# Performance work log

Hardware: AMD Instinct MI355X
Metric: run time of the kernel (lower is better)

## Reference

```python
import jax, jax.numpy as jnp
import numpy as np

N, E, F_IN, C, H12, H3, NCLS = 10000, 160000, 50, 256, 4, 6, 121


def gat_conv(x, src, dst, W, a_src, a_dst, b, heads, out_ch, concat, n):
    # x: [n, f_in]; W: [f_in, heads*out_ch]; a_*: [heads, out_ch]; src/dst: [e]
    h = (x @ W).reshape(n, heads, out_ch)
    # per-edge attention logits, LeakyReLU(0.2) as in PyG GATConv
    alpha = jax.nn.leaky_relu((h * a_src).sum(-1)[src] + (h * a_dst).sum(-1)[dst], 0.2)  # [e, heads]
    # segment softmax over incoming edges of each destination node
    amax = jax.ops.segment_max(alpha, dst, num_segments=n)
    ex = jnp.exp(alpha - amax[dst])
    denom = jax.ops.segment_sum(ex, dst, num_segments=n)
    w = ex / (denom[dst] + 1e-16)
    out = jax.ops.segment_sum(h[src] * w[..., None], dst, num_segments=n)  # [n, heads, out_ch]
    out = out.reshape(n, heads * out_ch) if concat else out.mean(axis=1)
    return out + b


def setup_inputs() -> dict:
    key = jax.random.key(0)
    ks = jax.random.split(key, 22)
    s = 0.05
    nrm = lambda k, shp: jax.random.normal(k, shp, jnp.float32) * s
    D = C * H12  # 1024
    return {
        "x": jax.random.normal(ks[0], (N, F_IN), jnp.float32),
        "edge_index": jax.random.randint(ks[1], (2, E), 0, N, dtype=jnp.int32),
        "W1": nrm(ks[2], (F_IN, H12 * C)), "a_src1": nrm(ks[3], (H12, C)), "a_dst1": nrm(ks[4], (H12, C)), "b1": jnp.zeros((H12 * C,), jnp.float32),
        "lW1": nrm(ks[5], (F_IN, D)), "lb1": jnp.zeros((D,), jnp.float32),
        "W2": nrm(ks[6], (D, H12 * C)), "a_src2": nrm(ks[7], (H12, C)), "a_dst2": nrm(ks[8], (H12, C)), "b2": jnp.zeros((H12 * C,), jnp.float32),
        "lW2": nrm(ks[9], (D, D)), "lb2": jnp.zeros((D,), jnp.float32),
        "W3": nrm(ks[10], (D, H3 * NCLS)), "a_src3": nrm(ks[11], (H3, NCLS)), "a_dst3": nrm(ks[12], (H3, NCLS)), "b3": jnp.zeros((NCLS,), jnp.float32),
        "lW3": nrm(ks[13], (D, NCLS)), "lb3": jnp.zeros((NCLS,), jnp.float32),
    }


def reference(x, edge_index, W1, a_src1, a_dst1, b1, lW1, lb1,
              W2, a_src2, a_dst2, b2, lW2, lb2,
              W3, a_src3, a_dst3, b3, lW3, lb3):
    n = x.shape[0]
    loop = jnp.arange(n, dtype=edge_index.dtype)  # self loops (PyG default)
    src = jnp.concatenate([edge_index[0], loop])
    dst = jnp.concatenate([edge_index[1], loop])
    h = jax.nn.elu(gat_conv(x, src, dst, W1, a_src1, a_dst1, b1, H12, C, True, n) + x @ lW1 + lb1)
    h = jax.nn.elu(gat_conv(h, src, dst, W2, a_src2, a_dst2, b2, H12, C, True, n) + h @ lW2 + lb2)
    return gat_conv(h, src, dst, W3, a_src3, a_dst3, b3, H3, NCLS, False, n) + h @ lW3 + lb3
```

## Files before the change

kernel.cpp:

```cpp
#include <hip/hip_runtime.h>
#include <cstdint>
#include <cstddef>

#define NN 10000
#define EE 160000
#define EN_ (EE + NN)
#define MPAD 10112
#define MT 79
#define CAP 128

typedef short s16x8 __attribute__((ext_vector_type(8)));
typedef float f32x4 __attribute__((ext_vector_type(4)));
typedef unsigned short u16;
typedef unsigned char u8;

__device__ __forceinline__ u16 f2bf(float f) {
  uint32_t u = __float_as_uint(f);
  uint32_t r = (u + 0x7fffu + ((u >> 16) & 1u)) >> 16;
  return (u16)r;
}
__device__ __forceinline__ float b2f(u16 u) {
  return __uint_as_float(((uint32_t)u) << 16);
}
__device__ __forceinline__ float b2f_lo(uint32_t p) { return __uint_as_float(p << 16); }
__device__ __forceinline__ float b2f_hi(uint32_t p) { return __uint_as_float(p & 0xffff0000u); }
__device__ __forceinline__ float lrelu02(float x) { return x > 0.f ? x : 0.2f * x; }
__device__ __forceinline__ float eluf(float x) { return x > 0.f ? x : (__expf(x) - 1.f); }
__device__ __forceinline__ u8 f2fp8(float v) {
  v = fminf(fmaxf(v, -448.f), 448.f);
  return (u8)(__builtin_amdgcn_cvt_pk_fp8_f32(v, v, 0, false) & 0xff);
}

__global__ void k_count(const int* __restrict__ ei, int* __restrict__ cnt) {
  int e = blockIdx.x * blockDim.x + threadIdx.x;
  if (e >= EN_) return;
  int d = (e < EE) ? ei[EE + e] : (e - EE);
  atomicAdd(&cnt[d], 1);
}

__global__ __launch_bounds__(1024) void k_scan(const int* __restrict__ cnt, int* __restrict__ off) {
  __shared__ int sums[1024];
  int t = threadIdx.x;
  const int per = (NN + 1023) / 1024;
  int base = t * per;
  int local = 0;
  for (int j = 0; j < per; ++j) {
    int idx = base + j;
    if (idx < NN) local += cnt[idx];
  }
  sums[t] = local;
  __syncthreads();
  for (int s = 1; s < 1024; s <<= 1) {
    int v = (t >= s) ? sums[t - s] : 0;
    __syncthreads();
    sums[t] += v;
    __syncthreads();
  }
  int run = (t == 0) ? 0 : sums[t - 1];
  for (int j = 0; j < per; ++j) {
    int idx = base + j;
    if (idx < NN) { off[idx] = run; run += cnt[idx]; }
  }
  if (t == 1023) off[NN] = EN_;
}

__global__ void k_fill(const int* __restrict__ ei, const int* __restrict__ off,
                       int* __restrict__ cursor, int* __restrict__ csr_src) {
  int e = blockIdx.x * blockDim.x + threadIdx.x;
  if (e >= EN_) return;
  int s, d;
  if (e < EE) { s = ei[e]; d = ei[EE + e]; } else { s = d = e - EE; }
  int p = atomicAdd(&cursor[d], 1);
  csr_src[off[d] + p] = s;
}

#define PREP_BLOCKS 3490
__global__ __launch_bounds__(256) void k_prep(
    const float* __restrict__ x, u16* __restrict__ xb,
    const float* __restrict__ W1, const float* __restrict__ lW1,
    const float* __restrict__ W2, const float* __restrict__ lW2,
    const float* __restrict__ W3, const float* __restrict__ lW3,
    u16* __restrict__ wtc1, u16* __restrict__ wtc2, u16* __restrict__ wtc3,
    const float* __restrict__ lb1, const float* __restrict__ lb2,
    const float* __restrict__ lb3, float* __restrict__ fb,
    u16* __restrict__ bufX, int* __restrict__ cnt) {
  int b = blockIdx.x, t = threadIdx.x;
  if (b < 768) {
    const float* W; u16* Bt; int K, N, Kpad, nb, kb;
    if (b < 16)       { W = W1;  Bt = wtc1;                       K = 50;   N = 1024; Kpad = 64;   nb = b;      kb = 0; }
    else if (b < 32)  { W = lW1; Bt = wtc1 + (size_t)1024 * 64;   K = 50;   N = 1024; Kpad = 64;   nb = b - 16; kb = 0; }
    else if (b < 288) { int r = b - 32;  W = W2;  Bt = wtc2;                         K = 1024; N = 1024; Kpad = 1024; nb = r & 15; kb = r >> 4; }
    else if (b < 544) { int r = b - 288; W = lW2; Bt = wtc2 + (size_t)1024 * 1024;   K = 1024; N = 1024; Kpad = 1024; nb = r & 15; kb = r >> 4; }
    else if (b < 736) { int r = b - 544; W = W3;  Bt = wtc3;                         K = 1024; N = 726;  Kpad = 1024; nb = r % 12; kb = r / 12; }
    else              { int r = b - 736; W = lW3; Bt = wtc3 + (size_t)768 * 1024;    K = 1024; N = 121;  Kpad = 1024; nb = r & 1;  kb = r >> 1; }
    __shared__ float tile[64][65];
    int kbase = kb * 64, nbase = nb * 64;
    int nl = t & 63, kl0 = t >> 6;
#pragma unroll
    for (int j = 0; j < 16; ++j) {
      int k = kbase + kl0 + j * 4, n = nbase + nl;
      tile[kl0 + j * 4][nl] = (k < K && n < N) ? W[(size_t)k * N + n] : 0.f;
    }
    __syncthreads();
    int nr = t >> 2, kc = (t & 3) * 16;
    uint32_t pk[8];
#pragma unroll
    for (int j = 0; j < 8; ++j) {
      pk[j] = (uint32_t)f2bf(tile[kc + 2 * j][nr]) | ((uint32_t)f2bf(tile[kc + 2 * j + 1][nr]) << 16);
    }
    uint4* dst = (uint4*)(Bt + (size_t)(nbase + nr) * Kpad + kbase + kc);
    dst[0] = make_uint4(pk[0], pk[1], pk[2], pk[3]);
    dst[1] = make_uint4(pk[4], pk[5], pk[6], pk[7]);
  } else if (b < 3296) {
    int idx = (b - 768) * 256 + t;
    if (idx < MPAD * 64) {
      int m = idx >> 6, k = idx & 63;
      xb[idx] = f2bf((m < NN && k < 50) ? x[m * 50 + k] : 0.f);
    }
  } else if (b < 3352) {
    int idx = (b - 3296) * 256 + t;
    ((uint4*)(bufX + (size_t)NN * 1024))[idx] = make_uint4(0, 0, 0, 0);
  } else if (b < 3470) {
    int idx = (b - 3352) * 256 + t;
    if (idx < 3 * NN + 1) cnt[idx] = 0;
  } else {
    int idx = (b - 3470) * 256 + t;
    if (idx < 4992) {
      float v = 0.f;
      if (idx < 2048)      { if (idx >= 1024) v = lb1[idx - 1024]; }
      else if (idx < 4096) { int j = idx - 2048; if (j >= 1024) v = lb2[j - 1024]; }
      else                 { int j = idx - 4096; if (j >= 768 && j < 889) v = lb3[j - 768]; }
      fb[idx] = v;
    }
  }
}

template <int OUT_S_BF16>
__global__ __launch_bounds__(256) void k_gemm_fused(
    const u16* __restrict__ A, const u16* __restrict__ Bt,
    const float* __restrict__ fbias,
    u8* __restrict__ outH, int ldH,
    void* __restrict__ outS, int ldS, int nsplit, int nrealS,
    int M, int Kpad, int NS) {
  __shared__ __align__(16) u16 lA[128 * 64];
  __shared__ __align__(16) u16 lB[128 * 64];
  int bid = blockIdx.x;
  int xcd = bid & 7, seq = bid >> 3;
  int nIdx = seq % NS, mloc = seq / NS;
  int mIdx = mloc * 8 + xcd;
  if (mIdx >= MT) return;
  int bm = mIdx * 128, bn = nIdx * 128;

  int t = threadIdx.x;
  int wave = t >> 6, lane = t & 63;
  int wm = (wave >> 1) * 64, wn = (wave & 1) * 64;

  f32x4 acc[4][4];
#pragma unroll
  for (int i = 0; i < 4; ++i)
#pragma unroll
    for (int j = 0; j < 4; ++j)
#pragma unroll
      for (int r = 0; r < 4; ++r) acc[i][j][r] = 0.f;

  int row = lane & 15, quad = lane >> 4;

  for (int k0 = 0; k0 < Kpad; k0 += 64) {
#pragma unroll
    for (int is = 0; is < 4; ++is) {
      int L = is * 256 + t;
      int m = L >> 3, c = L & 7;
      int j = c ^ (m & 7);
      const u16* gpA = A + (size_t)(bm + m) * Kpad + k0 + j * 8;
      const u16* gpB = Bt + (size_t)(bn + m) * Kpad + k0 + j * 8;
      u16* lpA = lA + (size_t)(is * 256 + wave * 64) * 8;
      u16* lpB = lB + (size_t)(is * 256 + wave * 64) * 8;
      __builtin_amdgcn_global_load_lds(
          (const __attribute__((address_space(1))) void*)gpA,
          (__attribute__((address_space(3))) void*)lpA, 16, 0, 0);
      __builtin_amdgcn_global_load_lds(
          (const __attribute__((address_space(1))) void*)gpB,
          (__attribute__((address_space(3))) void*)lpB, 16, 0, 0);
    }
    __syncthreads();

#pragma unroll
    for (int kk = 0; kk < 2; ++kk) {
      s16x8 af[4], bf[4];
#pragma unroll
      for (int mi = 0; mi < 4; ++mi) {
        int m = wm + mi * 16 + row;
        int c = (kk * 4 + quad) ^ (m & 7);
        af[mi] = *(const s16x8*)&lA[m * 64 + c * 8];
      }
#pragma unroll
      for (int ni = 0; ni < 4; ++ni) {
        int n = wn + ni * 16 + row;
        int c = (kk * 4 + quad) ^ (n & 7);
        bf[ni] = *(const s16x8*)&lB[n * 64 + c * 8];
      }
#pragma unroll
      for (int mi = 0; mi < 4; ++mi)
#pragma unroll
        for (int ni = 0; ni < 4; ++ni)
          acc[mi][ni] = __builtin_amdgcn_mfma_f32_16x16x32_bf16(af[mi], bf[ni], acc[mi][ni], 0, 0, 0);
    }
    __syncthreads();
  }

  int col = lane & 15, qr = (lane >> 4) * 4;
  bool isH = bn < nsplit;
#pragma unroll
  for (int mi = 0; mi < 4; ++mi) {
#pragma unroll
    for (int r = 0; r < 4; ++r) {
      int m = bm + wm + mi * 16 + qr + r;
      if (m >= M) continue;
#pragma unroll
      for (int ni = 0; ni < 4; ++ni) {
        int n = bn + wn + ni * 16 + col;
        float v = acc[mi][ni][r] + fbias[n];
        if (isH) {
          outH[(size_t)m * ldH + n] = f2fp8(v);
        } else {
          int c = n - nsplit;
          if (c < nrealS) {
            if (OUT_S_BF16) ((u16*)outS)[(size_t)m * ldS + c] = f2bf(v);
            else ((float*)outS)[(size_t)m * ldS + c] = v;
          }
        }
      }
    }
  }
}

__global__ void k_scores256(const u8* __restrict__ h, const float* __restrict__ a_src,
                            const float* __restrict__ a_dst, float* __restrict__ as_,
                            float* __restrict__ ad_) {
  int wid = (blockIdx.x * blockDim.x + threadIdx.x) >> 6;
  int lane = threadIdx.x & 63;
  if (wid >= NN * 4) return;
  int i = wid >> 2, hh = wid & 3;
  int pk = *(const int*)(h + (size_t)i * 1024 + hh * 256 + 4 * lane);
  float4 av = *(const float4*)(a_src + hh * 256 + 4 * lane);
  float4 dv = *(const float4*)(a_dst + hh * 256 + 4 * lane);
  float x0 = __builtin_amdgcn_cvt_f32_fp8(pk, 0);
  float x1 = __builtin_amdgcn_cvt_f32_fp8(pk, 1);
  float x2 = __builtin_amdgcn_cvt_f32_fp8(pk, 2);
  float x3 = __builtin_amdgcn_cvt_f32_fp8(pk, 3);
  float s1 = x0 * av.x + x1 * av.y + x2 * av.z + x3 * av.w;
  float s2 = x0 * dv.x + x1 * dv.y + x2 * dv.z + x3 * dv.w;
#pragma unroll
  for (int o = 32; o; o >>= 1) {
    s1 += __shfl_down(s1, o);
    s2 += __shfl_down(s2, o);
  }
  if (lane == 0) { as_[wid] = s1; ad_[wid] = s2; }
}

__global__ void k_scores(const u8* __restrict__ h, const float* __restrict__ a_src,
                         const float* __restrict__ a_dst, float* __restrict__ as_,
                         float* __restrict__ ad_, int H, int C, int ld) {
  int wid = (blockIdx.x * blockDim.x + threadIdx.x) >> 6;
  int lane = threadIdx.x & 63;
  if (wid >= NN * H) return;
  int i = wid / H, hh = wid - i * H;
  const u8* hp = h + (size_t)i * ld + hh * C;
  const float* sp = a_src + hh * C;
  const float* dp = a_dst + hh * C;
  float s1 = 0.f, s2 = 0.f;
  for (int c = lane; c < C; c += 64) {
    float v = __builtin_amdgcn_cvt_f32_fp8((int)hp[c], 0);
    s1 += v * sp[c];
    s2 += v * dp[c];
  }
#pragma unroll
  for (int o = 32; o; o >>= 1) {
    s1 += __shfl_down(s1, o);
    s2 += __shfl_down(s2, o);
  }
  if (lane == 0) { as_[wid] = s1; ad_[wid] = s2; }
}

__global__ __launch_bounds__(256) void k_agg_cat(
    const u8* __restrict__ h, const float* __restrict__ as_, const float* __restrict__ ad_,
    const int* __restrict__ off, const int* __restrict__ csr_src,
    const float* __restrict__ bias, const u16* __restrict__ skip, u16* __restrict__ outx) {
  const int F = 1024;
  int i = blockIdx.x, t = threadIdx.x;
  int start = off[i], end = off[i + 1];
  int wave = t >> 6, lane = t & 63;
  __shared__ int src_s[CAP];
  __shared__ float a_s[CAP][4];
  __shared__ float nm_s[4];
  float4 adv = *(const float4*)(ad_ + (size_t)i * 4);
  int hj = wave;
  float m_old = -1e30f;
  float denom = 0.f;
  float acc0 = 0.f, acc1 = 0.f, acc2 = 0.f, acc3 = 0.f;
  for (int e0 = start; e0 < end; e0 += CAP) {
    int ne = min(CAP, end - e0);
    __syncthreads();
    for (int j = t; j < ne; j += 256) {
      int s = csr_src[e0 + j];
      src_s[j] = s;
      float4 av = *(const float4*)(as_ + (size_t)s * 4);
      a_s[j][0] = lrelu02(av.x + adv.x);
      a_s[j][1] = lrelu02(av.y + adv.y);
      a_s[j][2] = lrelu02(av.z + adv.z);
      a_s[j][3] = lrelu02(av.w + adv.w);
    }
    __syncthreads();
    float cm = -1e30f;
    for (int j = lane; j < ne; j += 64) cm = fmaxf(cm, a_s[j][hj]);
#pragma unroll
    for (int o = 32; o; o >>= 1) cm = fmaxf(cm, __shfl_down(cm, o));
    if (lane == 0) nm_s[hj] = fmaxf(m_old, cm);
    __syncthreads();
    float nm0 = nm_s[0], nm1 = nm_s[1], nm2 = nm_s[2], nm3 = nm_s[3];
    for (int j = t; j < ne; j += 256) {
      a_s[j][0] = __expf(a_s[j][0] - nm0);
      a_s[j][1] = __expf(a_s[j][1] - nm1);
      a_s[j][2] = __expf(a_s[j][2] - nm2);
      a_s[j][3] = __expf(a_s[j][3] - nm3);
    }
    __syncthreads();
    float cd = 0.f;
    for (int j = lane; j < ne; j += 64) cd += a_s[j][hj];
#pragma unroll
    for (int o = 32; o; o >>= 1) cd += __shfl_down(cd, o);
    cd = __shfl(cd, 0);
    float nm = nm_s[hj];
    float rs = __expf(m_old - nm);
    acc0 *= rs; acc1 *= rs; acc2 *= rs; acc3 *= rs;
    denom = denom * rs + cd;
    m_old = nm;
#pragma unroll 4
    for (int e = 0; e < ne; ++e) {
      const u8* hp = h + (size_t)src_s[e] * F;
      int pk = *(const int*)(hp + 4 * t);
      float ww = a_s[e][hj];
      acc0 += ww * __builtin_amdgcn_cvt_f32_fp8(pk, 0);
      acc1 += ww * __builtin_amdgcn_cvt_f32_fp8(pk, 1);
      acc2 += ww * __builtin_amdgcn_cvt_f32_fp8(pk, 2);
      acc3 += ww * __builtin_amdgcn_cvt_f32_fp8(pk, 3);
    }
  }
  float rdm = 1.f / (denom + 1e-16f);
  int ch = 4 * t;
  float4 bb = *(const float4*)(bias + ch);
  uint2 sk = *(const uint2*)(skip + (size_t)i * F + ch);
  u16 o0 = f2bf(eluf(acc0 * rdm + bb.x + b2f_lo(sk.x)));
  u16 o1 = f2bf(eluf(acc1 * rdm + bb.y + b2f_hi(sk.x)));
  u16 o2 = f2bf(eluf(acc2 * rdm + bb.z + b2f_lo(sk.y)));
  u16 o3 = f2bf(eluf(acc3 * rdm + bb.w + b2f_hi(sk.y)));
  uint2 ov;
  ov.x = (uint32_t)o0 | ((uint32_t)o1 << 16);
  ov.y = (uint32_t)o2 | ((uint32_t)o3 << 16);
  *(uint2*)(outx + (size_t)i * F + ch) = ov;
}

__global__ __launch_bounds__(256) void k_agg_mean(
    const u8* __restrict__ h, const float* __restrict__ as_, const float* __restrict__ ad_,
    const int* __restrict__ off, const int* __restrict__ csr_src,
    const float* __restrict__ bias, float* __restrict__ out) {
  const int H = 6, C = 121, FP = 768;
  int i = blockIdx.x, t = threadIdx.x;
  int start = off[i], end = off[i + 1];
  int wave = t >> 6, lane = t & 63;
  __shared__ int src_s[CAP];
  __shared__ float a_s[CAP][H];
  __shared__ float nm_s[H], mo_s[H], d_s[H];
  __shared__ float agg_s[FP];
  float adv[H];
  {
    float2 v0 = *(const float2*)(ad_ + (size_t)i * H);
    float2 v1 = *(const float2*)(ad_ + (size_t)i * H + 2);
    float2 v2 = *(const float2*)(ad_ + (size_t)i * H + 4);
    adv[0] = v0.x; adv[1] = v0.y; adv[2] = v1.x; adv[3] = v1.y; adv[4] = v2.x; adv[5] = v2.y;
  }
  if (t < H) { mo_s[t] = -1e30f; d_s[t] = 0.f; }
  int c0 = 4 * t;
  bool act = t < 192;
  int hd[4];
#pragma unroll
  for (int r = 0; r < 4; ++r) {
    int c = c0 + r;
    hd[r] = (act && c < 726) ? (c / C) : 0;
  }
  float acc[4] = {0.f, 0.f, 0.f, 0.f};
  for (int e0 = start; e0 < end; e0 += CAP) {
    int ne = min(CAP, end - e0);
    __syncthreads();
    for (int j = t; j < ne; j += 256) {
      int s = csr_src[e0 + j];
      src_s[j] = s;
      float2 v0 = *(const float2*)(as_ + (size_t)s * H);
      float2 v1 = *(const float2*)(as_ + (size_t)s * H + 2);
      float2 v2 = *(const float2*)(as_ + (size_t)s * H + 4);
      a_s[j][0] = lrelu02(v0.x + adv[0]);
      a_s[j][1] = lrelu02(v0.y + adv[1]);
      a_s[j][2] = lrelu02(v1.x + adv[2]);
      a_s[j][3] = lrelu02(v1.y + adv[3]);
      a_s[j][4] = lrelu02(v2.x + adv[4]);
      a_s[j][5] = lrelu02(v2.y + adv[5]);
    }
    __syncthreads();
    for (int hh = wave; hh < H; hh += 4) {
      float cm = -1e30f;
      for (int j = lane; j < ne; j += 64) cm = fmaxf(cm, a_s[j][hh]);
#pragma unroll
      for (int o = 32; o; o >>= 1) cm = fmaxf(cm, __shfl_down(cm, o));
      if (lane == 0) nm_s[hh] = fmaxf(mo_s[hh], cm);
    }
    __syncthreads();
#pragma unroll
    for (int r = 0; r < 4; ++r) acc[r] *= __expf(mo_s[hd[r]] - nm_s[hd[r]]);
    for (int j = t; j < ne; j += 256) {
#pragma unroll
      for (int hh = 0; hh < H; ++hh) a_s[j][hh] = __expf(a_s[j][hh] - nm_s[hh]);
    }
    __syncthreads();
    for (int hh = wave; hh < H; hh += 4) {
      float cd = 0.f;
      for (int j = lane; j < ne; j += 64) cd += a_s[j][hh];
#pragma unroll
      for (int o = 32; o; o >>= 1) cd += __shfl_down(cd, o);
      if (lane == 0) {
        d_s[hh] = d_s[hh] * __expf(mo_s[hh] - nm_s[hh]) + cd;
        mo_s[hh] = nm_s[hh];
      }
    }
    if (act) {
#pragma unroll 4
      for (int e = 0; e < ne; ++e) {
        const u8* hp = h + (size_t)src_s[e] * FP;
        int pk = *(const int*)(hp + c0);
        acc[0] += a_s[e][hd[0]] * __builtin_amdgcn_cvt_f32_fp8(pk, 0);
        acc[1] += a_s[e][hd[1]] * __builtin_amdgcn_cvt_f32_fp8(pk, 1);
        acc[2] += a_s[e][hd[2]] * __builtin_amdgcn_cvt_f32_fp8(pk, 2);
        acc[3] += a_s[e][hd[3]] * __builtin_amdgcn_cvt_f32_fp8(pk, 3);
      }
    }
  }
  __syncthreads();
  if (act) {
#pragma unroll
    for (int r = 0; r < 4; ++r) agg_s[c0 + r] = acc[r] / (d_s[hd[r]] + 1e-16f);
  }
  __syncthreads();
  if (t < C) {
    float s = 0.f;
#pragma unroll
    for (int hh = 0; hh < H; ++hh) s += agg_s[hh * C + t];
    size_t idx = (size_t)i * C + t;
    out[idx] += s * (1.f / 6.f) + bias[t];
  }
}

extern "C" void kernel_launch(void* const* d_in, const int* in_sizes, int n_in,
                              void* d_out, int out_size, void* d_ws, size_t ws_size,
                              hipStream_t stream) {
  const float* x = (const float*)d_in[0];
  const int* ei = (const int*)d_in[1];
  const float* W1 = (const float*)d_in[2];
  const float* a_src1 = (const float*)d_in[3];
  const float* a_dst1 = (const float*)d_in[4];
  const float* b1 = (const float*)d_in[5];
  const float* lW1 = (const float*)d_in[6];
  const float* lb1 = (const float*)d_in[7];
  const float* W2 = (const float*)d_in[8];
  const float* a_src2 = (const float*)d_in[9];
  const float* a_dst2 = (const float*)d_in[10];
  const float* b2 = (const float*)d_in[11];
  const float* lW2 = (const float*)d_in[12];
  const float* lb2 = (const float*)d_in[13];
  const float* W3 = (const float*)d_in[14];
  const float* a_src3 = (const float*)d_in[15];
  const float* a_dst3 = (const float*)d_in[16];
  const float* b3 = (const float*)d_in[17];
  const float* lW3 = (const float*)d_in[18];
  const float* lb3 = (const float*)d_in[19];
  float* outp = (float*)d_out;

  char* ws = (char*)d_ws;
  size_t o = 0;
  auto alloc = [&](size_t bytes) { void* p = ws + o; o += (bytes + 255) & ~(size_t)255; return p; };
  u8* bufH8 = (u8*)alloc((size_t)MPAD * 1024);
  u16* bufX = (u16*)alloc((size_t)MPAD * 1024 * 2);
  u16* bufS = (u16*)alloc((size_t)NN * 1024 * 2);
  u16* xb16 = (u16*)alloc((size_t)MPAD * 64 * 2);
  u16* wtc1 = (u16*)alloc((size_t)2048 * 64 * 2);
  u16* wtc2 = (u16*)alloc((size_t)2048 * 1024 * 2);
  u16* wtc3 = (u16*)alloc((size_t)896 * 1024 * 2);
  float* fb12 = (float*)alloc((size_t)4992 * 4);
  float* fb1 = fb12;
  float* fb2 = fb12 + 2048;
  float* fb3 = fb12 + 4096;
  float* as_ = (float*)alloc((size_t)NN * 6 * 4);
  float* ad_ = (float*)alloc((size_t)NN * 6 * 4);
  int* cnt = (int*)alloc((size_t)(3 * NN + 1) * 4);
  int* offs = cnt + NN;
  int* cursor = offs + NN + 1;
  int* csr_src = (int*)alloc((size_t)EN_ * 4);

  k_prep<<<PREP_BLOCKS, 256, 0, stream>>>(x, xb16, W1, lW1, W2, lW2, W3, lW3,
                                          wtc1, wtc2, wtc3, lb1, lb2, lb3, fb12,
                                          bufX, cnt);
  int eb = (EN_ + 255) / 256;
  k_count<<<eb, 256, 0, stream>>>(ei, cnt);
  k_scan<<<1, 1024, 0, stream>>>(cnt, offs);
  k_fill<<<eb, 256, 0, stream>>>(ei, offs, cursor, csr_src);

  {
    k_gemm_fused<1><<<16 * 80, 256, 0, stream>>>(
        xb16, wtc1, fb1, bufH8, 1024, bufS, 1024, 1024, 1024, NN, 64, 16);
    k_scores256<<<10000, 256, 0, stream>>>(bufH8, a_src1, a_dst1, as_, ad_);
    k_agg_cat<<<NN, 256, 0, stream>>>(bufH8, as_, ad_, offs, csr_src, b1, bufS, bufX);
  }
  {
    k_gemm_fused<1><<<16 * 80, 256, 0, stream>>>(
        bufX, wtc2, fb2, bufH8, 1024, bufS, 1024, 1024, 1024, NN, 1024, 16);
    k_scores256<<<10000, 256, 0, stream>>>(bufH8, a_src2, a_dst2, as_, ad_);
    k_agg_cat<<<NN, 256, 0, stream>>>(bufH8, as_, ad_, offs, csr_src, b2, bufS, bufX);
  }
  {
    k_gemm_fused<0><<<7 * 80, 256, 0, stream>>>(
        bufX, wtc3, fb3, bufH8, 768, outp, 121, 768, 121, NN, 1024, 7);
    k_scores<<<(NN * 6 + 3) / 4, 256, 0, stream>>>(bufH8, a_src3, a_dst3, as_, ad_, 6, 121, 768);
    k_agg_mean<<<NN, 256, 0, stream>>>(bufH8, as_, ad_, offs, csr_src, b3, outp);
  }
}
```

Measured before the change: 402.0 us.

## Fuse attention score dot products into GEMM epilogue and streamline softmax aggregation

```diff
diff --git a/kernel.cpp b/kernel.cpp
--- a/kernel.cpp
+++ b/kernel.cpp
@@ -18,9 +18,6 @@
   uint32_t u = __float_as_uint(f);
   uint32_t r = (u + 0x7fffu + ((u >> 16) & 1u)) >> 16;
   return (u16)r;
-}
-__device__ __forceinline__ float b2f(u16 u) {
-  return __uint_as_float(((uint32_t)u) << 16);
 }
 __device__ __forceinline__ float b2f_lo(uint32_t p) { return __uint_as_float(p << 16); }
 __device__ __forceinline__ float b2f_hi(uint32_t p) { return __uint_as_float(p & 0xffff0000u); }
@@ -74,7 +71,7 @@
   csr_src[off[d] + p] = s;
 }
 
-#define PREP_BLOCKS 3490
+#define PREP_BLOCKS 3647
 __global__ __launch_bounds__(256) void k_prep(
     const float* __restrict__ x, u16* __restrict__ xb,
     const float* __restrict__ W1, const float* __restrict__ lW1,
@@ -83,7 +80,7 @@
     u16* __restrict__ wtc1, u16* __restrict__ wtc2, u16* __restrict__ wtc3,
     const float* __restrict__ lb1, const float* __restrict__ lb2,
     const float* __restrict__ lb3, float* __restrict__ fb,
-    u16* __restrict__ bufX, int* __restrict__ cnt) {
+    u16* __restrict__ bufX, int* __restrict__ cnt, float* __restrict__ asad) {
   int b = blockIdx.x, t = threadIdx.x;
   if (b < 768) {
     const float* W; u16* Bt; int K, N, Kpad, nb, kb;
@@ -123,7 +120,7 @@
   } else if (b < 3470) {
     int idx = (b - 3352) * 256 + t;
     if (idx < 3 * NN + 1) cnt[idx] = 0;
-  } else {
+  } else if (b < 3490) {
     int idx = (b - 3470) * 256 + t;
     if (idx < 4992) {
       float v = 0.f;
@@ -132,6 +129,9 @@
       else                 { int j = idx - 4096; if (j >= 768 && j < 889) v = lb3[j - 768]; }
       fb[idx] = v;
     }
+  } else {
+    int idx = (b - 3490) * 256 + t;
+    if (idx < 40000) ((uint4*)asad)[idx] = make_uint4(0, 0, 0, 0);
   }
 }
 
@@ -141,7 +141,9 @@
     const float* __restrict__ fbias,
     u8* __restrict__ outH, int ldH,
     void* __restrict__ outS, int ldS, int nsplit, int nrealS,
-    int M, int Kpad, int NS) {
+    int M, int Kpad, int NS,
+    const float* __restrict__ aS, const float* __restrict__ aD,
+    float* __restrict__ asO, float* __restrict__ adO) {
   __shared__ __align__(16) u16 lA[128 * 64];
   __shared__ __align__(16) u16 lB[128 * 64];
   int bid = blockIdx.x;
@@ -210,52 +212,52 @@
 
   int col = lane & 15, qr = (lane >> 4) * 4;
   bool isH = bn < nsplit;
+  int head = (bn + wn) >> 8;
 #pragma unroll
   for (int mi = 0; mi < 4; ++mi) {
 #pragma unroll
     for (int r = 0; r < 4; ++r) {
       int m = bm + wm + mi * 16 + qr + r;
       if (m >= M) continue;
-#pragma unroll
-      for (int ni = 0; ni < 4; ++ni) {
-        int n = bn + wn + ni * 16 + col;
-        float v = acc[mi][ni][r] + fbias[n];
-        if (isH) {
-          outH[(size_t)m * ldH + n] = f2fp8(v);
-        } else {
-          int c = n - nsplit;
+      float vv[4];
+#pragma unroll
+      for (int ni = 0; ni < 4; ++ni)
+        vv[ni] = acc[mi][ni][r] + fbias[bn + wn + ni * 16 + col];
+      if (isH) {
+#pragma unroll
+        for (int ni = 0; ni < 4; ++ni)
+          outH[(size_t)m * ldH + (bn + wn + ni * 16 + col)] = f2fp8(vv[ni]);
+        if (asO) {
+          float s1 = 0.f, s2 = 0.f;
+#pragma unroll
+          for (int ni = 0; ni < 4; ++ni) {
+            int n = bn + wn + ni * 16 + col;
+            s1 += vv[ni] * aS[n];
+            s2 += vv[ni] * aD[n];
+          }
+#pragma unroll
+          for (int msk = 8; msk; msk >>= 1) {
+            s1 += __shfl_xor(s1, msk);
+            s2 += __shfl_xor(s2, msk);
+          }
+          if (col == 0) {
+            atomicAdd(&asO[(size_t)m * 4 + head], s1);
+            atomicAdd(&adO[(size_t)m * 4 + head], s2);
+          }
+        }
+      } else {
+        int c0 = bn + wn - nsplit;
+#pragma unroll
+        for (int ni = 0; ni < 4; ++ni) {
+          int c = c0 + ni * 16 + col;
           if (c < nrealS) {
-            if (OUT_S_BF16) ((u16*)outS)[(size_t)m * ldS + c] = f2bf(v);
-            else ((float*)outS)[(size_t)m * ldS + c] = v;
+            if (OUT_S_BF16) ((u16*)outS)[(size_t)m * ldS + c] = f2bf(vv[ni]);
+            else ((float*)outS)[(size_t)m * ldS + c] = vv[ni];
           }
         }
       }
     }
   }
-}
-
-__global__ void k_scores256(const u8* __restrict__ h, const float* __restrict__ a_src,
-                            const float* __restrict__ a_dst, float* __restrict__ as_,
-                            float* __restrict__ ad_) {
-  int wid = (blockIdx.x * blockDim.x + threadIdx.x) >> 6;
-  int lane = threadIdx.x & 63;
-  if (wid >= NN * 4) return;
-  int i = wid >> 2, hh = wid & 3;
-  int pk = *(const int*)(h + (size_t)i * 1024 + hh * 256 + 4 * lane);
-  float4 av = *(const float4*)(a_src + hh * 256 + 4 * lane);
-  float4 dv = *(const float4*)(a_dst + hh * 256 + 4 * lane);
-  float x0 = __builtin_amdgcn_cvt_f32_fp8(pk, 0);
-  float x1 = __builtin_amdgcn_cvt_f32_fp8(pk, 1);
-  float x2 = __builtin_amdgcn_cvt_f32_fp8(pk, 2);
-  float x3 = __builtin_amdgcn_cvt_f32_fp8(pk, 3);
-  float s1 = x0 * av.x + x1 * av.y + x2 * av.z + x3 * av.w;
-  float s2 = x0 * dv.x + x1 * dv.y + x2 * dv.z + x3 * dv.w;
-#pragma unroll
-  for (int o = 32; o; o >>= 1) {
-    s1 += __shfl_down(s1, o);
-    s2 += __shfl_down(s2, o);
-  }
-  if (lane == 0) { as_[wid] = s1; ad_[wid] = s2; }
 }
 
 __global__ void k_scores(const u8* __restrict__ h, const float* __restrict__ a_src,
@@ -292,54 +294,43 @@
   int wave = t >> 6, lane = t & 63;
   __shared__ int src_s[CAP];
   __shared__ float a_s[CAP][4];
-  __shared__ float nm_s[4];
   float4 adv = *(const float4*)(ad_ + (size_t)i * 4);
-  int hj = wave;
-  float m_old = -1e30f;
-  float denom = 0.f;
+  float m_run = -1e30f, denom = 0.f;
   float acc0 = 0.f, acc1 = 0.f, acc2 = 0.f, acc3 = 0.f;
   for (int e0 = start; e0 < end; e0 += CAP) {
     int ne = min(CAP, end - e0);
-    __syncthreads();
-    for (int j = t; j < ne; j += 256) {
-      int s = csr_src[e0 + j];
-      src_s[j] = s;
+    if (e0 > start) __syncthreads();
+    if (t < ne) {
+      int s = csr_src[e0 + t];
+      src_s[t] = s;
       float4 av = *(const float4*)(as_ + (size_t)s * 4);
-      a_s[j][0] = lrelu02(av.x + adv.x);
-      a_s[j][1] = lrelu02(av.y + adv.y);
-      a_s[j][2] = lrelu02(av.z + adv.z);
-      a_s[j][3] = lrelu02(av.w + adv.w);
+      a_s[t][0] = lrelu02(av.x + adv.x);
+      a_s[t][1] = lrelu02(av.y + adv.y);
+      a_s[t][2] = lrelu02(av.z + adv.z);
+      a_s[t][3] = lrelu02(av.w + adv.w);
     }
     __syncthreads();
     float cm = -1e30f;
-    for (int j = lane; j < ne; j += 64) cm = fmaxf(cm, a_s[j][hj]);
-#pragma unroll
-    for (int o = 32; o; o >>= 1) cm = fmaxf(cm, __shfl_down(cm, o));
-    if (lane == 0) nm_s[hj] = fmaxf(m_old, cm);
-    __syncthreads();
-    float nm0 = nm_s[0], nm1 = nm_s[1], nm2 = nm_s[2], nm3 = nm_s[3];
-    for (int j = t; j < ne; j += 256) {
-      a_s[j][0] = __expf(a_s[j][0] - nm0);
-      a_s[j][1] = __expf(a_s[j][1] - nm1);
-      a_s[j][2] = __expf(a_s[j][2] - nm2);
-      a_s[j][3] = __expf(a_s[j][3] - nm3);
-    }
-    __syncthreads();
-    float cd = 0.f;
-    for (int j = lane; j < ne; j += 64) cd += a_s[j][hj];
-#pragma unroll
-    for (int o = 32; o; o >>= 1) cd += __shfl_down(cd, o);
-    cd = __shfl(cd, 0);
-    float nm = nm_s[hj];
-    float rs = __expf(m_old - nm);
+    for (int j = lane; j < ne; j += 64) cm = fmaxf(cm, a_s[j][wave]);
+#pragma unroll
+    for (int msk = 32; msk; msk >>= 1) cm = fmaxf(cm, __shfl_xor(cm, msk));
+    float nm = fmaxf(m_run, cm);
+    float sm = 0.f;
+    for (int j = lane; j < ne; j += 64) {
+      float e = __expf(a_s[j][wave] - nm);
+      a_s[j][wave] = e;
+      sm += e;
+    }
+#pragma unroll
+    for (int msk = 32; msk; msk >>= 1) sm += __shfl_xor(sm, msk);
+    float rs = __expf(m_run - nm);
     acc0 *= rs; acc1 *= rs; acc2 *= rs; acc3 *= rs;
-    denom = denom * rs + cd;
-    m_old = nm;
+    denom = denom * rs + sm;
+    m_run = nm;
 #pragma unroll 4
     for (int e = 0; e < ne; ++e) {
-      const u8* hp = h + (size_t)src_s[e] * F;
-      int pk = *(const int*)(hp + 4 * t);
-      float ww = a_s[e][hj];
+      int pk = *(const int*)(h + (size_t)src_s[e] * F + 4 * t);
+      float ww = a_s[e][wave];
       acc0 += ww * __builtin_amdgcn_cvt_f32_fp8(pk, 0);
       acc1 += ww * __builtin_amdgcn_cvt_f32_fp8(pk, 1);
       acc2 += ww * __builtin_amdgcn_cvt_f32_fp8(pk, 2);
@@ -370,7 +361,7 @@
   int wave = t >> 6, lane = t & 63;
   __shared__ int src_s[CAP];
   __shared__ float a_s[CAP][H];
-  __shared__ float nm_s[H], mo_s[H], d_s[H];
+  __shared__ float nm_s[H], sm_s[H];
   __shared__ float agg_s[FP];
   float adv[H];
   {
@@ -379,7 +370,6 @@
     float2 v2 = *(const float2*)(ad_ + (size_t)i * H + 4);
     adv[0] = v0.x; adv[1] = v0.y; adv[2] = v1.x; adv[3] = v1.y; adv[4] = v2.x; adv[5] = v2.y;
   }
-  if (t < H) { mo_s[t] = -1e30f; d_s[t] = 0.f; }
   int c0 = 4 * t;
   bool act = t < 192;
   int hd[4];
@@ -389,64 +379,69 @@
     hd[r] = (act && c < 726) ? (c / C) : 0;
   }
   float acc[4] = {0.f, 0.f, 0.f, 0.f};
+  float m_r[4] = {-1e30f, -1e30f, -1e30f, -1e30f};
+  float d_r[4] = {0.f, 0.f, 0.f, 0.f};
   for (int e0 = start; e0 < end; e0 += CAP) {
     int ne = min(CAP, end - e0);
-    __syncthreads();
-    for (int j = t; j < ne; j += 256) {
-      int s = csr_src[e0 + j];
-      src_s[j] = s;
+    if (e0 > start) __syncthreads();
+    if (t < ne) {
+      int s = csr_src[e0 + t];
+      src_s[t] = s;
       float2 v0 = *(const float2*)(as_ + (size_t)s * H);
       float2 v1 = *(const float2*)(as_ + (size_t)s * H + 2);
       float2 v2 = *(const float2*)(as_ + (size_t)s * H + 4);
-      a_s[j][0] = lrelu02(v0.x + adv[0]);
-      a_s[j][1] = lrelu02(v0.y + adv[1]);
-      a_s[j][2] = lrelu02(v1.x + adv[2]);
-      a_s[j][3] = lrelu02(v1.y + adv[3]);
-      a_s[j][4] = lrelu02(v2.x + adv[4]);
-      a_s[j][5] = lrelu02(v2.y + adv[5]);
+      a_s[t][0] = lrelu02(v0.x + adv[0]);
+      a_s[t][1] = lrelu02(v0.y + adv[1]);
+      a_s[t][2] = lrelu02(v1.x + adv[2]);
+      a_s[t][3] = lrelu02(v1.y + adv[3]);
+      a_s[t][4] = lrelu02(v2.x + adv[4]);
+      a_s[t][5] = lrelu02(v2.y + adv[5]);
     }
     __syncthreads();
     for (int hh = wave; hh < H; hh += 4) {
       float cm = -1e30f;
       for (int j = lane; j < ne; j += 64) cm = fmaxf(cm, a_s[j][hh]);
 #pragma unroll
-      for (int o = 32; o; o >>= 1) cm = fmaxf(cm, __shfl_down(cm, o));
-      if (lane == 0) nm_s[hh] = fmaxf(mo_s[hh], cm);
-    }
-    __syncthreads();
-#pragma unroll
-    for (int r = 0; r < 4; ++r) acc[r] *= __expf(mo_s[hd[r]] - nm_s[hd[r]]);
-    for (int j = t; j < ne; j += 256) {
-#pragma unroll
-      for (int hh = 0; hh < H; ++hh) a_s[j][hh] = __expf(a_s[j][hh] - nm_s[hh]);
-    }
-    __syncthreads();
-    for (int hh = wave; hh < H; hh += 4) {
-      float cd = 0.f;
-      for (int j = lane; j < ne; j += 64) cd += a_s[j][hh];
-#pragma unroll
-      for (int o = 32; o; o >>= 1) cd += __shfl_down(cd, o);
-      if (lane == 0) {
-        d_s[hh] = d_s[hh] * __expf(mo_s[hh] - nm_s[hh]) + cd;
-        mo_s[hh] = nm_s[hh];
+      for (int msk = 32; msk; msk >>= 1) cm = fmaxf(cm, __shfl_xor(cm, msk));
+      float sm = 0.f;
+      for (int j = lane; j < ne; j += 64) {
+        float e = __expf(a_s[j][hh] - cm);
+        a_s[j][hh] = e;
+        sm += e;
       }
-    }
+#pragma unroll
+      for (int msk = 32; msk; msk >>= 1) sm += __shfl_xor(sm, msk);
+      if (lane == 0) { nm_s[hh] = cm; sm_s[hh] = sm; }
+    }
+    __syncthreads();
     if (act) {
+#pragma unroll
+      for (int r = 0; r < 4; ++r) {
+        float cm = nm_s[hd[r]];
+        float nm = fmaxf(m_r[r], cm);
+        float rs_old = __expf(m_r[r] - nm);
+        float rs_new = __expf(cm - nm);
+        acc[r] *= rs_old;
+        d_r[r] = d_r[r] * rs_old + sm_s[hd[r]] * rs_new;
+        m_r[r] = nm;
+        acc[r] += 0.f;
+        adv[r] = rs_new;
+      }
 #pragma unroll 4
       for (int e = 0; e < ne; ++e) {
         const u8* hp = h + (size_t)src_s[e] * FP;
         int pk = *(const int*)(hp + c0);
-        acc[0] += a_s[e][hd[0]] * __builtin_amdgcn_cvt_f32_fp8(pk, 0);
-        acc[1] += a_s[e][hd[1]] * __builtin_amdgcn_cvt_f32_fp8(pk, 1);
-        acc[2] += a_s[e][hd[2]] * __builtin_amdgcn_cvt_f32_fp8(pk, 2);
-        acc[3] += a_s[e][hd[3]] * __builtin_amdgcn_cvt_f32_fp8(pk, 3);
+        acc[0] += adv[0] * a_s[e][hd[0]] * __builtin_amdgcn_cvt_f32_fp8(pk, 0);
+        acc[1] += adv[1] * a_s[e][hd[1]] * __builtin_amdgcn_cvt_f32_fp8(pk, 1);
+        acc[2] += adv[2] * a_s[e][hd[2]] * __builtin_amdgcn_cvt_f32_fp8(pk, 2);
+        acc[3] += adv[3] * a_s[e][hd[3]] * __builtin_amdgcn_cvt_f32_fp8(pk, 3);
       }
     }
   }
   __syncthreads();
   if (act) {
 #pragma unroll
-    for (int r = 0; r < 4; ++r) agg_s[c0 + r] = acc[r] / (d_s[hd[r]] + 1e-16f);
+    for (int r = 0; r < 4; ++r) agg_s[c0 + r] = acc[r] / (d_r[r] + 1e-16f);
   }
   __syncthreads();
   if (t < C) {
@@ -497,8 +492,10 @@
   float* fb1 = fb12;
   float* fb2 = fb12 + 2048;
   float* fb3 = fb12 + 4096;
-  float* as_ = (float*)alloc((size_t)NN * 6 * 4);
-  float* ad_ = (float*)alloc((size_t)NN * 6 * 4);
+  float* asad = (float*)alloc((size_t)160000 * 4);
+  float* as1 = asad, *ad1 = asad + 40000, *as2 = asad + 80000, *ad2 = asad + 120000;
+  float* as3 = (float*)alloc((size_t)NN * 6 * 4);
+  float* ad3 = (float*)alloc((size_t)NN * 6 * 4);
   int* cnt = (int*)alloc((size_t)(3 * NN + 1) * 4);
   int* offs = cnt + NN;
   int* cursor = offs + NN + 1;
@@ -506,7 +503,7 @@
 
   k_prep<<<PREP_BLOCKS, 256, 0, stream>>>(x, xb16, W1, lW1, W2, lW2, W3, lW3,
                                           wtc1, wtc2, wtc3, lb1, lb2, lb3, fb12,
-                                          bufX, cnt);
+                                          bufX, cnt, asad);
   int eb = (EN_ + 255) / 256;
   k_count<<<eb, 256, 0, stream>>>(ei, cnt);
   k_scan<<<1, 1024, 0, stream>>>(cnt, offs);
@@ -514,20 +511,21 @@
 
   {
     k_gemm_fused<1><<<16 * 80, 256, 0, stream>>>(
-        xb16, wtc1, fb1, bufH8, 1024, bufS, 1024, 1024, 1024, NN, 64, 16);
-    k_scores256<<<10000, 256, 0, stream>>>(bufH8, a_src1, a_dst1, as_, ad_);
-    k_agg_cat<<<NN, 256, 0, stream>>>(bufH8, as_, ad_, offs, csr_src, b1, bufS, bufX);
+        xb16, wtc1, fb1, bufH8, 1024, bufS, 1024, 1024, 1024, NN, 64, 16,
+        a_src1, a_dst1, as1, ad1);
+    k_agg_cat<<<NN, 256, 0, stream>>>(bufH8, as1, ad1, offs, csr_src, b1, bufS, bufX);
   }
   {
     k_gemm_fused<1><<<16 * 80, 256, 0, stream>>>(
-        bufX, wtc2, fb2, bufH8, 1024, bufS, 1024, 1024, 1024, NN, 1024, 16);
-    k_scores256<<<10000, 256, 0, stream>>>(bufH8, a_src2, a_dst2, as_, ad_);
-    k_agg_cat<<<NN, 256, 0, stream>>>(bufH8, as_, ad_, offs, csr_src, b2, bufS, bufX);
+        bufX, wtc2, fb2, bufH8, 1024, bufS, 1024, 1024, 1024, NN, 1024, 16,
+        a_src2, a_dst2, as2, ad2);
+    k_agg_cat<<<NN, 256, 0, stream>>>(bufH8, as2, ad2, offs, csr_src, b2, bufS, bufX);
   }
   {
     k_gemm_fused<0><<<7 * 80, 256, 0, stream>>>(
-        bufX, wtc3, fb3, bufH8, 768, outp, 121, 768, 121, NN, 1024, 7);
-    k_scores<<<(NN * 6 + 3) / 4, 256, 0, stream>>>(bufH8, a_src3, a_dst3, as_, ad_, 6, 121, 768);
-    k_agg_mean<<<NN, 256, 0, stream>>>(bufH8, as_, ad_, offs, csr_src, b3, outp);
-  }
-}
+        bufX, wtc3, fb3, bufH8, 768, outp, 121, 768, 121, NN, 1024, 7,
+        nullptr, nullptr, nullptr, nullptr);
+    k_scores<<<(NN * 6 + 3) / 4, 256, 0, stream>>>(bufH8, a_src3, a_dst3, as3, ad3, 6, 121, 768);
+    k_agg_mean<<<NN, 256, 0, stream>>>(bufH8, as3, ad3, offs, csr_src, b3, outp);
+  }
+}
```

Result: no change. 409.2 us (+1.8%).
